# Performance work log

Measured on AMD Instinct MI355X. Metric: run time of the kernel, lower is better.

Reference implementation:

```python
import jax, jax.numpy as jnp
import numpy as np

B, T, C = 4, 1024, 1024
H, G = 16, 1            # n_head, n_query_groups
D = C // H              # head_dim = 64
E, K = 4, 1             # moe_num_experts, moe_k
FF = 4 * C              # ffn/expert hidden = 4096
EPS = 1e-5


def setup_inputs() -> dict:
    key = jax.random.key(0)
    ks = jax.random.split(key, 24)
    w = lambda k, shape: (jax.random.normal(k, shape, jnp.float32) * 0.02)
    return {
        "x": jax.random.normal(ks[0], (B, T, C), jnp.float32),
        # attention (torch Linear weights stored as [in, out])
        "wq": w(ks[1], (C, C)), "wk": w(ks[2], (C, C)), "wv": w(ks[3], (C, C)),
        "wo": w(ks[4], (C, C)), "bo": jnp.zeros((C,), jnp.float32),
        # feedforward
        "ff_w1": w(ks[5], (C, FF)), "ff_b1": jnp.zeros((FF,), jnp.float32),
        "ff_w2": w(ks[6], (FF, C)), "ff_b2": jnp.zeros((C,), jnp.float32),
        # MoE experts (stacked) + gate
        "exp_w1": w(ks[7], (E, C, FF)), "exp_b1": jnp.zeros((E, FF), jnp.float32),
        "exp_w2": w(ks[8], (E, FF, C)), "exp_b2": jnp.zeros((E, C), jnp.float32),
        "gate_w": w(ks[9], (C, E)), "gate_b": jnp.zeros((E,), jnp.float32),
        # layernorms
        "ln1_g": jnp.ones((C,), jnp.float32), "ln1_b": jnp.zeros((C,), jnp.float32),
        "ln2_g": jnp.ones((C,), jnp.float32), "ln2_b": jnp.zeros((C,), jnp.float32),
        "ln3_g": jnp.ones((C,), jnp.float32), "ln3_b": jnp.zeros((C,), jnp.float32),
    }


def _ln(x, g, b):
    m = x.mean(-1, keepdims=True)
    v = x.var(-1, keepdims=True)
    return (x - m) / jnp.sqrt(v + EPS) * g + b


def reference(x, wq, wk, wv, wo, bo, ff_w1, ff_b1, ff_w2, ff_b2,
              exp_w1, exp_b1, exp_w2, exp_b2, gate_w, gate_b,
              ln1_g, ln1_b, ln2_g, ln2_b, ln3_g, ln3_b):
    Hg = H // G
    # ---- grouped-query causal self-attention ----
    h = _ln(x, ln1_g, ln1_b)
    # [B,T,C] -> [B,G,Hg,T,D]
    q = (h @ wq).reshape(B, T, G, Hg, D).transpose(0, 2, 3, 1, 4)
    k = (h @ wk).reshape(B, T, G, Hg, D).transpose(0, 2, 3, 1, 4)
    v = (h @ wv).reshape(B, T, G, Hg, D).transpose(0, 2, 3, 1, 4)
    scores = jnp.einsum('bghtd,bghsd->bghts', q, k) / np.float32(np.sqrt(D))
    causal = jnp.tril(jnp.ones((T, T), bool))
    scores = jnp.where(causal, scores, -jnp.inf)
    probs = jax.nn.softmax(scores, axis=-1)
    o = jnp.einsum('bghts,bghsd->bghtd', probs, v)          # [B,G,Hg,T,D]
    o = o.reshape(B, H, T, D).transpose(0, 2, 1, 3).reshape(B, T, C)
    x = x + o @ wo + bo
    # ---- dense feedforward ----
    h = _ln(x, ln2_g, ln2_b)
    x = x + jax.nn.relu(h @ ff_w1 + ff_b1) @ ff_w2 + ff_b2
    # ---- MoE: compute ALL experts densely, gather top-k (faithful to source) ----
    h = _ln(x, ln3_g, ln3_b)
    gate = h @ gate_w + gate_b                               # [B,T,E]
    topk_s, topk_i = jax.lax.top_k(gate, K)                  # [B,T,K]
    topk_w = jax.nn.softmax(topk_s, axis=-1)
    hidden = jax.nn.relu(jnp.einsum('btc,ech->bteh', h, exp_w1) + exp_b1)
    expert_out = jnp.einsum('bteh,ehc->btec', hidden, exp_w2) + exp_b2  # [B,T,E,C]
    sel = jnp.take_along_axis(expert_out, topk_i[..., None], axis=2)    # [B,T,K,C]
    moe = (sel * topk_w[..., None]).sum(axis=2)
    return x + moe
```

## Files before the change

### kernel.cpp

```cpp
#include <hip/hip_runtime.h>


using f16   = _Float16;
using f16x4 = __attribute__((ext_vector_type(4))) _Float16;
using f16x8 = __attribute__((ext_vector_type(8))) _Float16;
using f32x4 = __attribute__((ext_vector_type(4))) float;

__device__ __forceinline__ void async16(void* l, const void* g) {
  __builtin_amdgcn_global_load_lds(
      (const __attribute__((address_space(1))) unsigned*)g,
      (__attribute__((address_space(3))) unsigned*)l, 16, 0, 0);
}

template <bool SPLITW>
__global__ __launch_bounds__(256) void transpose_k(
    const float* __restrict__ in, f16* __restrict__ oh, f16* __restrict__ ol,
    int R, int Cc) {
  const size_t bofs = (size_t)blockIdx.y * R * Cc;
  in += bofs; oh += bofs;
  if constexpr (SPLITW) ol += bofs;
  __shared__ float tile[32][33];
  const int nbx = Cc >> 5;
  const int bx = blockIdx.x % nbx, by = blockIdx.x / nbx;
  const int tx = threadIdx.x & 31, ty = threadIdx.x >> 5;
#pragma unroll
  for (int i = 0; i < 4; ++i) {
    int r = ty + i * 8;
    tile[r][tx] = in[(size_t)(by * 32 + r) * Cc + bx * 32 + tx];
  }
  __syncthreads();
#pragma unroll
  for (int i = 0; i < 4; ++i) {
    int oc = ty + i * 8;
    float v = tile[tx][oc];
    size_t o = (size_t)(bx * 32 + oc) * R + by * 32 + tx;
    f16 hi = (f16)v;
    oh[o] = hi;
    if constexpr (SPLITW) ol[o] = (f16)(v - (float)hi);
  }
}

__global__ __launch_bounds__(256) void ln_k(
    const float* __restrict__ x, const float* __restrict__ g,
    const float* __restrict__ b, f16* __restrict__ outh, f16* __restrict__ outl) {
  const int row = blockIdx.x;
  const float4 vv = ((const float4*)(x + (size_t)row * 1024))[threadIdx.x];
  float s = vv.x + vv.y + vv.z + vv.w;
  float sq = vv.x * vv.x + vv.y * vv.y + vv.z * vv.z + vv.w * vv.w;
#pragma unroll
  for (int mm = 32; mm; mm >>= 1) { s += __shfl_xor(s, mm); sq += __shfl_xor(sq, mm); }
  __shared__ float red[8];
  const int wv = threadIdx.x >> 6;
  if ((threadIdx.x & 63) == 0) { red[wv] = s; red[4 + wv] = sq; }
  __syncthreads();
  s = red[0] + red[1] + red[2] + red[3];
  sq = red[4] + red[5] + red[6] + red[7];
  const float mean = s * 0.0009765625f;
  const float rstd = rsqrtf(sq * 0.0009765625f - mean * mean + 1e-5f);
  const int c = threadIdx.x * 4;
  const float xs[4] = {vv.x, vv.y, vv.z, vv.w};
  f16x4 ovh, ovl;
#pragma unroll
  for (int i = 0; i < 4; ++i) {
    float val = (xs[i] - mean) * rstd * g[c + i] + b[c + i];
    f16 hi = (f16)val;
    ovh[i] = hi;
    ovl[i] = (f16)(val - (float)hi);
  }
  *(f16x4*)(outh + (size_t)row * 1024 + c) = ovh;
  *(f16x4*)(outl + (size_t)row * 1024 + c) = ovl;
}

__global__ __launch_bounds__(256) void gate_k(
    const float* __restrict__ x, const float* __restrict__ g, const float* __restrict__ b,
    const float* __restrict__ gw, const float* __restrict__ gb,
    int* __restrict__ cnt, int* __restrict__ idxAll, int* __restrict__ eid) {
  const int t = blockIdx.x;
  const float4 vv = ((const float4*)(x + (size_t)t * 1024))[threadIdx.x];
  float s = vv.x + vv.y + vv.z + vv.w;
  float sq = vv.x * vv.x + vv.y * vv.y + vv.z * vv.z + vv.w * vv.w;
#pragma unroll
  for (int mm = 32; mm; mm >>= 1) { s += __shfl_xor(s, mm); sq += __shfl_xor(sq, mm); }
  __shared__ float red[8];
  __shared__ float redv[4][4];
  const int wv = threadIdx.x >> 6;
  if ((threadIdx.x & 63) == 0) { red[wv] = s; red[4 + wv] = sq; }
  __syncthreads();
  s = red[0] + red[1] + red[2] + red[3];
  sq = red[4] + red[5] + red[6] + red[7];
  const float mean = s * 0.0009765625f;
  const float rstd = rsqrtf(sq * 0.0009765625f - mean * mean + 1e-5f);
  const int c = threadIdx.x * 4;
  const float xs[4] = {vv.x, vv.y, vv.z, vv.w};
  float a0 = 0.f, a1 = 0.f, a2 = 0.f, a3 = 0.f;
#pragma unroll
  for (int i = 0; i < 4; ++i) {
    float ln = (xs[i] - mean) * rstd * g[c + i] + b[c + i];
    const float4 w4 = ((const float4*)gw)[c + i];
    a0 += ln * w4.x; a1 += ln * w4.y; a2 += ln * w4.z; a3 += ln * w4.w;
  }
#pragma unroll
  for (int mm = 32; mm; mm >>= 1) {
    a0 += __shfl_xor(a0, mm); a1 += __shfl_xor(a1, mm);
    a2 += __shfl_xor(a2, mm); a3 += __shfl_xor(a3, mm);
  }
  if ((threadIdx.x & 63) == 0) {
    redv[wv][0] = a0; redv[wv][1] = a1; redv[wv][2] = a2; redv[wv][3] = a3;
  }
  __syncthreads();
  if (threadIdx.x == 0) {
    float ge[4];
#pragma unroll
    for (int e = 0; e < 4; ++e)
      ge[e] = redv[0][e] + redv[1][e] + redv[2][e] + redv[3][e] + gb[e];
    int be = 0; float bvv = ge[0];
#pragma unroll
    for (int e = 1; e < 4; ++e) if (ge[e] > bvv) { bvv = ge[e]; be = e; }
    int pos = atomicAdd(&cnt[be], 1);
    idxAll[(be << 12) + pos] = t;
    eid[t] = be;
  }
}

__global__ void init_moe(int* cnt) { if (threadIdx.x < 4) cnt[threadIdx.x] = 0; }

#define MAXMT 36
__global__ void plan_k(const int* __restrict__ cnt, int* __restrict__ desc) {
  if (threadIdx.x == 0) {
    int t = 0;
    for (int e = 0; e < 4; ++e) {
      const int c = cnt[e];
      for (int m = 0; m < c; m += 128) desc[t++] = (e << 16) | (m >> 7);
    }
    for (; t < MAXMT; ++t) desc[t] = -1;
  }
}

template <bool MOE>
__global__ __launch_bounds__(256) void reduce_k(
    const float* __restrict__ p0, const float* __restrict__ p1,
    const float* __restrict__ res, const float* __restrict__ bias,
    const int* __restrict__ eid, float* __restrict__ o) {
  const int row = blockIdx.x, t = threadIdx.x;
  const float* bp = MOE ? bias + (size_t)eid[row] * 1024 : bias;
  const float4 a = ((const float4*)(p0 + (size_t)row * 1024))[t];
  const float4 b = ((const float4*)(p1 + (size_t)row * 1024))[t];
  const float4 r = ((const float4*)(res + (size_t)row * 1024))[t];
  const float4 bb = ((const float4*)bp)[t];
  float4 o4;
  o4.x = r.x + a.x + b.x + bb.x;
  o4.y = r.y + a.y + b.y + bb.y;
  o4.z = r.z + a.z + b.z + bb.z;
  o4.w = r.w + a.w + b.w + bb.w;
  ((float4*)(o + (size_t)row * 1024))[t] = o4;
}

template <bool SPLIT, bool RELU, bool BIAS, bool RES, bool GATHER, int OUT,
          bool QKV3, bool KSPLIT>
__global__ __launch_bounds__(256, 2) void gemm_k(
    const f16* __restrict__ Ah, const f16* __restrict__ Al,
    const f16* __restrict__ Bh, const f16* __restrict__ Bl,
    float* __restrict__ outf, float* __restrict__ outf2,
    f16* __restrict__ outh, f16* __restrict__ outl,
    const float* __restrict__ bias, const float* __restrict__ res,
    const int* __restrict__ idxAll, const int* __restrict__ cntAll,
    const int* __restrict__ desc,
    int M, int N, int K) {
  const int NB = N >> 7;
  int m0, n0, ks = 0;
  int cnt = M;
  const int* idx = nullptr;
  if constexpr (GATHER) {
    int rem = blockIdx.x;
    if constexpr (KSPLIT) {
      const int half = (int)gridDim.x >> 1;
      ks = rem >= half; rem -= ks * half;
    }
    const int mt = rem / NB, nt = rem - mt * NB;
    const int d = desc[mt];
    if (d < 0) return;
    const int e = d >> 16;
    m0 = (d & 0xffff) << 7;
    n0 = nt << 7;
    cnt = cntAll[e];
    idx = idxAll + (e << 12);
    Bh += (size_t)e * N * K;
    if (BIAS) bias += (size_t)e * N;
  } else {
    int rem = blockIdx.x;
    const int ntile = (int)gridDim.x >> (KSPLIT ? 1 : 0);
    if constexpr (KSPLIT) { ks = rem >= ntile; rem -= ks * ntile; }
    const int q2 = ntile >> 3;
    const int bid = (rem & 7) * q2 + (rem >> 3);
    m0 = (bid / NB) << 7; n0 = (bid % NB) << 7;
  }

  __shared__ __align__(16) char lds[65536];

  const int tid = threadIdx.x;
  const int wave = tid >> 6, lane = tid & 63;
  const int wr = (wave >> 1) << 6, wc = (wave & 1) << 6;
  const int srow = lane >> 3;
  const int lc = (lane & 7) ^ srow;
  const int kofs = (SPLIT ? (lc >> 1) : lc) << 4;

  const int kshift = (KSPLIT && ks) ? (K >> 1) : 0;

  const char* srcA[4];
  const char* srcB[4];
#pragma unroll
  for (int s = 0; s < 4; ++s) {
    const int tr = (wave * 4 + s) * 8 + srow;
    int gm = m0 + tr;
    if constexpr (GATHER) gm = idx[gm < cnt ? gm : cnt - 1];
    const f16* baseA = (SPLIT && (lc & 1)) ? Al : Ah;
    srcA[s] = (const char*)baseA + ((size_t)gm * K + kshift) * 2 + kofs;
    const f16* baseB = (SPLIT && (lc & 1)) ? Bl : Bh;
    srcB[s] = (const char*)baseB + ((size_t)(n0 + tr) * K + kshift) * 2 + kofs;
  }
  char* const ldsw = lds + wave * 4096;

  const int s4 = lane >> 4, l7 = lane & 7, fr = lane & 15;
  int offAh[4], offAl[4], offBh[4], offBl[4];
#pragma unroll
  for (int i = 0; i < 4; ++i) {
    const int row = wr + i * 16 + fr;
    const int col = wc + i * 16 + fr;
    if constexpr (SPLIT) {
      offAh[i] = row * 128 + (((2 * s4) ^ l7) << 4);
      offAl[i] = row * 128 + (((2 * s4 + 1) ^ l7) << 4);
      offBh[i] = 16384 + col * 128 + (((2 * s4) ^ l7) << 4);
      offBl[i] = 16384 + col * 128 + (((2 * s4 + 1) ^ l7) << 4);
    } else {
      offAh[i] = row * 128 + ((s4 ^ l7) << 4);
      offAl[i] = row * 128 + (((4 + s4) ^ l7) << 4);
      offBh[i] = 16384 + col * 128 + ((s4 ^ l7) << 4);
      offBl[i] = 16384 + col * 128 + (((4 + s4) ^ l7) << 4);
    }
  }

  f32x4 acc[4][4] = {};

  constexpr int KSTEP = SPLIT ? 32 : 64;
  const int nt_ = (KSPLIT ? (K >> 1) : K) / KSTEP;

#pragma unroll
  for (int s = 0; s < 4; ++s) {
    async16(ldsw + s * 1024, srcA[s]);
    async16(ldsw + 16384 + s * 1024, srcB[s]);
  }

  for (int t = 0; t < nt_; ++t) {
    const int cur = t & 1;
    if (t + 1 < nt_) {
      const size_t kb = (size_t)(t + 1) * (KSTEP * 2);
      char* dst = ldsw + (cur ^ 1) * 32768;
#pragma unroll
      for (int s = 0; s < 4; ++s) {
        async16(dst + s * 1024, srcA[s] + kb);
        async16(dst + 16384 + s * 1024, srcB[s] + kb);
      }
      asm volatile("s_waitcnt vmcnt(8)" ::: "memory");
    } else {
      asm volatile("s_waitcnt vmcnt(0)" ::: "memory");
    }
    __builtin_amdgcn_s_barrier();
    __builtin_amdgcn_sched_barrier(0);

    const char* cab = lds + cur * 32768;
    f16x8 va[4], vb[4], va2[4], vb2[4];
#pragma unroll
    for (int i = 0; i < 4; ++i) {
      va[i]  = *(const f16x8*)(cab + offAh[i]);
      va2[i] = *(const f16x8*)(cab + offAl[i]);
      vb[i]  = *(const f16x8*)(cab + offBh[i]);
      vb2[i] = *(const f16x8*)(cab + offBl[i]);
    }
    __builtin_amdgcn_s_setprio(1);
#pragma unroll
    for (int i = 0; i < 4; ++i)
#pragma unroll
      for (int j = 0; j < 4; ++j) {
        if constexpr (SPLIT) {
          acc[i][j] = __builtin_amdgcn_mfma_f32_16x16x32_f16(va[i],  vb[j],  acc[i][j], 0, 0, 0);
          acc[i][j] = __builtin_amdgcn_mfma_f32_16x16x32_f16(va2[i], vb[j],  acc[i][j], 0, 0, 0);
          acc[i][j] = __builtin_amdgcn_mfma_f32_16x16x32_f16(va[i],  vb2[j], acc[i][j], 0, 0, 0);
        } else {
          acc[i][j] = __builtin_amdgcn_mfma_f32_16x16x32_f16(va[i],  vb[j],  acc[i][j], 0, 0, 0);
          acc[i][j] = __builtin_amdgcn_mfma_f32_16x16x32_f16(va2[i], vb2[j], acc[i][j], 0, 0, 0);
        }
      }
    __builtin_amdgcn_s_setprio(0);
    __builtin_amdgcn_sched_barrier(0);
    __builtin_amdgcn_s_barrier();
  }

  const int cl = lane & 15, rg = lane >> 4;
  float* const po = (OUT == 3) ? (ks ? outf2 : outf) : outf;
#pragma unroll
  for (int i = 0; i < 4; ++i) {
#pragma unroll
    for (int r = 0; r < 4; ++r) {
      const int mloc = m0 + wr + i * 16 + rg * 4 + r;
      if (GATHER && mloc >= cnt) continue;
      const int orow = GATHER ? idx[mloc] : mloc;
#pragma unroll
      for (int j = 0; j < 4; ++j) {
        const int col = n0 + wc + j * 16 + cl;
        float v2 = acc[i][j][r];
        if (BIAS) v2 += bias[col];
        if (RELU) v2 = v2 > 0.f ? v2 : 0.f;
        if (RES) v2 += res[(size_t)orow * N + col];
        size_t oidx;
        if constexpr (QKV3) {
          if (col < 2048) {
            oidx = ((size_t)(col >> 10) * M + orow) * 1024 + (col & 1023);
          } else {
            const int c = col - 2048;
            oidx = (size_t)2 * M * 1024 +
                   (((size_t)(orow >> 10) * 16 + (c >> 6)) * 64 + (c & 63)) * 1024 +
                   (orow & 1023);
          }
        } else {
          oidx = (size_t)orow * N + col;
        }
        if constexpr (OUT == 0 || OUT == 3) {
          po[oidx] = v2;
        } else if constexpr (OUT == 1) {
          f16 hi = (f16)v2;
          outh[oidx] = hi;
          outl[oidx] = (f16)(v2 - (float)hi);
        } else {
          outh[oidx] = (f16)v2;
        }
      }
    }
  }
}

__global__ __launch_bounds__(256, 3) void attn_k(
    const f16* __restrict__ qh, const f16* __restrict__ ql,
    const f16* __restrict__ kh, const f16* __restrict__ kl,
    const f16* __restrict__ vth, const f16* __restrict__ vtl,
    f16* __restrict__ oh, f16* __restrict__ ol) {
  const int qt = 15 - (blockIdx.x & 15), hd = (blockIdx.x >> 4) & 15, bb = blockIdx.x >> 8;
  const int tid = threadIdx.x, wave = tid >> 6, lane = tid & 63;
  __shared__ __align__(16) char QPs[16384], Ks[16384], Vs[16384];
  const int swz = (((lane & 7) ^ ((lane >> 3) & 7)) << 4);
  const size_t tok0 = (size_t)bb * 1024;
  const int hoff = hd * 64;
  const size_t vbase = ((size_t)(bb * 16 + hd) * 64) * 1024;
  const float L2E = 1.44269504089f;

#pragma unroll
  for (int r = 0; r < 2; ++r) {
    const int chunk = wave * 2 + r;
    const int row = chunk * 8 + (lane >> 3);
    const size_t byte = (((tok0 + qt * 64 + row) * 1024 + hoff) << 1) + swz;
    async16(QPs + chunk * 1024, (const char*)qh + byte);
    async16(QPs + 8192 + chunk * 1024, (const char*)ql + byte);
  }
  __syncthreads();
  f16x8 qr_h[2], qr_l[2];
#pragma unroll
  for (int ks = 0; ks < 2; ++ks) {
    const int qrow = wave * 16 + (lane & 15);
    const int qoff = qrow * 128 + ((((ks << 2) + (lane >> 4)) ^ (qrow & 7)) << 4);
    qr_h[ks] = *(const f16x8*)(QPs + qoff);
    qr_l[ks] = *(const f16x8*)(QPs + 8192 + qoff);
  }

  f32x4 oacc[4] = {};
  float mrun[4] = {-1e30f, -1e30f, -1e30f, -1e30f};
  float lrun[4] = {};

  for (int kt = 0; kt <= qt; ++kt) {
    __syncthreads();
#pragma unroll
    for (int r = 0; r < 2; ++r) {
      const int chunk = wave * 2 + r;
      const int row = chunk * 8 + (lane >> 3);
      const size_t kbyte = (((tok0 + kt * 64 + row) * 1024 + hoff) << 1) + swz;
      async16(Ks + chunk * 1024, (const char*)kh + kbyte);
      async16(Ks + 8192 + chunk * 1024, (const char*)kl + kbyte);
      const size_t vbyte = (((vbase + (size_t)row * 1024) + kt * 64) << 1) + swz;
      async16(Vs + chunk * 1024, (const char*)vth + vbyte);
      async16(Vs + 8192 + chunk * 1024, (const char*)vtl + vbyte);
    }
    __syncthreads();

    f32x4 s[4] = {};
#pragma unroll
    for (int ks = 0; ks < 2; ++ks) {
#pragma unroll
      for (int j = 0; j < 4; ++j) {
        const int col = j * 16 + (lane & 15);
        const int koff = col * 128 + ((((ks << 2) + (lane >> 4)) ^ (col & 7)) << 4);
        f16x8 b_h = *(const f16x8*)(Ks + koff);
        f16x8 b_l = *(const f16x8*)(Ks + 8192 + koff);
        s[j] = __builtin_amdgcn_mfma_f32_16x16x32_f16(qr_h[ks], b_h, s[j], 0, 0, 0);
        s[j] = __builtin_amdgcn_mfma_f32_16x16x32_f16(qr_l[ks], b_h, s[j], 0, 0, 0);
        s[j] = __builtin_amdgcn_mfma_f32_16x16x32_f16(qr_h[ks], b_l, s[j], 0, 0, 0);
      }
    }

    const bool diag = (kt == qt);
    float pmax[4] = {-1e30f, -1e30f, -1e30f, -1e30f};
#pragma unroll
    for (int j = 0; j < 4; ++j)
#pragma unroll
      for (int r = 0; r < 4; ++r) {
        float sv = s[j][r] * 0.125f;
        if (diag) {
          const int qloc = wave * 16 + (lane >> 4) * 4 + r;
          const int kvl = j * 16 + (lane & 15);
          if (kvl > qloc) sv = -1e30f;
        }
        s[j][r] = sv;
        pmax[r] = fmaxf(pmax[r], sv);
      }
    char* pbh = QPs + wave * 2048;
    char* pbl = QPs + 8192 + wave * 2048;
#pragma unroll
    for (int r = 0; r < 4; ++r) {
#pragma unroll
      for (int mm = 1; mm < 16; mm <<= 1)
        pmax[r] = fmaxf(pmax[r], __shfl_xor(pmax[r], mm, 16));
      const float mnew = fmaxf(mrun[r], pmax[r]);
      const float al = exp2f((mrun[r] - mnew) * L2E);
      mrun[r] = mnew;
      lrun[r] *= al;
      oacc[0][r] *= al; oacc[1][r] *= al; oacc[2][r] *= al; oacc[3][r] *= al;
    }

    float psum[4] = {};
#pragma unroll
    for (int j = 0; j < 4; ++j)
#pragma unroll
      for (int r = 0; r < 4; ++r) {
        const float p = exp2f((s[j][r] - mrun[r]) * L2E);
        psum[r] += p;
        const int lr = (lane >> 4) * 4 + r;
        const int kvl = j * 16 + (lane & 15);
        const int poff = lr * 128 + ((kvl * 2) ^ ((lr & 7) << 4));
        f16 ph = (f16)p;
        *(f16*)(pbh + poff) = ph;
        *(f16*)(pbl + poff) = (f16)(p - (float)ph);
      }
#pragma unroll
    for (int r = 0; r < 4; ++r) {
#pragma unroll
      for (int mm = 1; mm < 16; mm <<= 1)
        psum[r] += __shfl_xor(psum[r], mm, 16);
      lrun[r] += psum[r];
    }

#pragma unroll
    for (int ks = 0; ks < 2; ++ks) {
      const int prow = lane & 15;
      const int poff = prow * 128 + ((((ks << 2) + (lane >> 4)) ^ (prow & 7)) << 4);
      f16x8 a_h = *(const f16x8*)(pbh + poff);
      f16x8 a_l = *(const f16x8*)(pbl + poff);
#pragma unroll
      for (int jd = 0; jd < 4; ++jd) {
        const int col = jd * 16 + (lane & 15);
        const int voff = col * 128 + ((((ks << 2) + (lane >> 4)) ^ (col & 7)) << 4);
        f16x8 b_h = *(const f16x8*)(Vs + voff);
        f16x8 b_l = *(const f16x8*)(Vs + 8192 + voff);
        oacc[jd] = __builtin_amdgcn_mfma_f32_16x16x32_f16(a_h, b_h, oacc[jd], 0, 0, 0);
        oacc[jd] = __builtin_amdgcn_mfma_f32_16x16x32_f16(a_l, b_h, oacc[jd], 0, 0, 0);
        oacc[jd] = __builtin_amdgcn_mfma_f32_16x16x32_f16(a_h, b_l, oacc[jd], 0, 0, 0);
      }
    }
  }

#pragma unroll
  for (int r = 0; r < 4; ++r) {
    const float inv = 1.0f / lrun[r];
    const size_t trow = tok0 + qt * 64 + wave * 16 + (lane >> 4) * 4 + r;
#pragma unroll
    for (int jd = 0; jd < 4; ++jd) {
      const int col = hoff + jd * 16 + (lane & 15);
      const float val = oacc[jd][r] * inv;
      const f16 hi = (f16)val;
      oh[trow * 1024 + col] = hi;
      ol[trow * 1024 + col] = (f16)(val - (float)hi);
    }
  }
}

extern "C" void kernel_launch(void* const* d_in, const int* in_sizes, int n_in,
                              void* d_out, int out_size, void* d_ws, size_t ws_size,
                              hipStream_t stream) {
  const float* x0   = (const float*)d_in[0];
  const float* wq   = (const float*)d_in[1];
  const float* wk   = (const float*)d_in[2];
  const float* wv   = (const float*)d_in[3];
  const float* wo   = (const float*)d_in[4];
  const float* bo   = (const float*)d_in[5];
  const float* ffw1 = (const float*)d_in[6];
  const float* ffb1 = (const float*)d_in[7];
  const float* ffw2 = (const float*)d_in[8];
  const float* ffb2 = (const float*)d_in[9];
  const float* ew1  = (const float*)d_in[10];
  const float* eb1  = (const float*)d_in[11];
  const float* ew2  = (const float*)d_in[12];
  const float* eb2  = (const float*)d_in[13];
  const float* gw   = (const float*)d_in[14];
  const float* gb   = (const float*)d_in[15];
  const float* l1g  = (const float*)d_in[16];
  const float* l1b  = (const float*)d_in[17];
  const float* l2g  = (const float*)d_in[18];
  const float* l2b  = (const float*)d_in[19];
  const float* l3g  = (const float*)d_in[20];
  const float* l3b  = (const float*)d_in[21];
  float* out = (float*)d_out;

  char* w = (char*)d_ws;
  const size_t M1 = (size_t)1024 * 1024;
  const size_t A1 = (size_t)4096 * 1024 * 2;
  const size_t W4 = (size_t)1024 * 4096 * 2;
  f16* wqkvh = (f16*)w; w += 3 * M1 * 2;
  f16* wqkvl = (f16*)w; w += 3 * M1 * 2;
  f16* woh = (f16*)w; w += M1 * 2;
  f16* wol = (f16*)w; w += M1 * 2;
  f16* f1h = (f16*)w; w += W4;  f16* f1l = (f16*)w; w += W4;
  f16* f2h = (f16*)w; w += W4;  f16* f2l = (f16*)w; w += W4;
  f16* e1t = (f16*)w; w += 4 * W4;
  f16* e2t = (f16*)w; w += 4 * W4;
  f16* hh  = (f16*)w; w += A1;  f16* hl  = (f16*)w; w += A1;
  f16* qkv_h = (f16*)w; w += 3 * A1;
  f16* qkv_l = (f16*)w; w += 3 * A1;
  f16* o_h = (f16*)w; w += A1;  f16* o_l = (f16*)w; w += A1;
  float* x1 = (float*)w; w += (size_t)4096 * 1024 * 4;
  int* cnt = (int*)w; w += 256;
  int* idx = (int*)w; w += (size_t)4 * 4096 * 4;
  int* eid = (int*)w; w += (size_t)4096 * 4;
  int* desc = (int*)w; w += 256;
  f16* hid_h = qkv_h;
  f16* hid_l = (f16*)((char*)qkv_h + (((size_t)32) << 20));
  f16* ffh   = qkv_h;
  float* pW0 = (float*)hh;
  float* pW1 = (float*)qkv_h;
  float* pF0 = (float*)wqkvh;
  float* pF1 = (float*)hh;
  float* pM0 = (float*)((char*)qkv_l + (((size_t)8) << 20));
  float* pM1 = (float*)o_h;

  transpose_k<true><<<1024, 256, 0, stream>>>(wq, wqkvh, wqkvl, 1024, 1024);
  transpose_k<true><<<1024, 256, 0, stream>>>(wk, wqkvh + M1, wqkvl + M1, 1024, 1024);
  transpose_k<true><<<1024, 256, 0, stream>>>(wv, wqkvh + 2 * M1, wqkvl + 2 * M1, 1024, 1024);
  transpose_k<true><<<1024, 256, 0, stream>>>(wo, woh, wol, 1024, 1024);
  transpose_k<true><<<4096, 256, 0, stream>>>(ffw1, f1h, f1l, 1024, 4096);
  transpose_k<true><<<4096, 256, 0, stream>>>(ffw2, f2h, f2l, 4096, 1024);
  transpose_k<false><<<dim3(4096, 4), 256, 0, stream>>>(ew1, e1t, nullptr, 1024, 4096);
  transpose_k<false><<<dim3(4096, 4), 256, 0, stream>>>(ew2, e2t, nullptr, 4096, 1024);

  const size_t TOK = (size_t)4096 * 1024;
  ln_k<<<4096, 256, 0, stream>>>(x0, l1g, l1b, hh, hl);
  gemm_k<true, false, false, false, false, 1, true, false><<<768, 256, 0, stream>>>(
      hh, hl, wqkvh, wqkvl, nullptr, nullptr, qkv_h, qkv_l,
      nullptr, nullptr, nullptr, nullptr, nullptr, 4096, 3072, 1024);
  attn_k<<<1024, 256, 0, stream>>>(qkv_h, qkv_l, qkv_h + TOK, qkv_l + TOK,
                                   qkv_h + 2 * TOK, qkv_l + 2 * TOK, o_h, o_l);
  gemm_k<true, false, false, false, false, 3, false, true><<<512, 256, 0, stream>>>(
      o_h, o_l, woh, wol, pW0, pW1, nullptr, nullptr,
      nullptr, nullptr, nullptr, nullptr, nullptr, 4096, 1024, 1024);
  reduce_k<false><<<4096, 256, 0, stream>>>(pW0, pW1, x0, bo, nullptr, x1);

  ln_k<<<4096, 256, 0, stream>>>(x1, l2g, l2b, hh, hl);
  gemm_k<true, true, true, false, false, 1, false, false><<<1024, 256, 0, stream>>>(
      hh, hl, f1h, f1l, nullptr, nullptr, hid_h, hid_l,
      ffb1, nullptr, nullptr, nullptr, nullptr, 4096, 4096, 1024);
  gemm_k<true, false, false, false, false, 3, false, true><<<512, 256, 0, stream>>>(
      hid_h, hid_l, f2h, f2l, pF0, pF1, nullptr, nullptr,
      nullptr, nullptr, nullptr, nullptr, nullptr, 4096, 1024, 4096);
  reduce_k<false><<<4096, 256, 0, stream>>>(pF0, pF1, x1, ffb2, nullptr, out);

  ln_k<<<4096, 256, 0, stream>>>(out, l3g, l3b, hh, hl);
  init_moe<<<1, 64, 0, stream>>>(cnt);
  gate_k<<<4096, 256, 0, stream>>>(out, l3g, l3b, gw, gb, cnt, idx, eid);
  plan_k<<<1, 64, 0, stream>>>(cnt, desc);
  gemm_k<false, true, true, false, true, 2, false, false><<<MAXMT * 32, 256, 0, stream>>>(
      hh, nullptr, e1t, nullptr, nullptr, nullptr, ffh, nullptr,
      eb1, nullptr, idx, cnt, desc, 4096, 4096, 1024);
  gemm_k<false, false, false, false, true, 3, false, true><<<2 * MAXMT * 8, 256, 0, stream>>>(
      ffh, nullptr, e2t, nullptr, pM0, pM1, nullptr, nullptr,
      nullptr, nullptr, idx, cnt, desc, 4096, 1024, 4096);
  reduce_k<true><<<4096, 256, 0, stream>>>(pM0, pM1, out, eb2, eid, out);
}
```

Baseline: 793.1 us.

## Drop GEMM LDS double buffering to single buffer for higher occupancy

Removes the double-buffered async prefetch in the GEMM main loop and uses one 32 KB LDS buffer, loading each K-step and syncing before compute. Launch bounds rise to 4 blocks per CU so more waves can hide memory latency instead of software pipelining. The trade-off is losing overlap of global loads with MFMA within a block. It also relies on __syncthreads waiting for the global_load_lds transfers, which the removed explicit vmcnt waits used to guarantee, and 4 blocks of 256 threads may not fit under the register budget.

```diff
diff --git a/kernel.cpp b/kernel.cpp
--- a/kernel.cpp
+++ b/kernel.cpp
@@ -157,7 +157,7 @@
 
 template <bool SPLIT, bool RELU, bool BIAS, bool RES, bool GATHER, int OUT,
           bool QKV3, bool KSPLIT>
-__global__ __launch_bounds__(256, 2) void gemm_k(
+__global__ __launch_bounds__(256, 4) void gemm_k(
     const f16* __restrict__ Ah, const f16* __restrict__ Al,
     const f16* __restrict__ Bh, const f16* __restrict__ Bl,
     float* __restrict__ outf, float* __restrict__ outf2,
@@ -195,7 +195,7 @@
     m0 = (bid / NB) << 7; n0 = (bid % NB) << 7;
   }
 
-  __shared__ __align__(16) char lds[65536];
+  __shared__ __align__(16) char lds[32768];
 
   const int tid = threadIdx.x;
   const int wave = tid >> 6, lane = tid & 63;
@@ -244,37 +244,22 @@
   constexpr int KSTEP = SPLIT ? 32 : 64;
   const int nt_ = (KSPLIT ? (K >> 1) : K) / KSTEP;
 
-#pragma unroll
-  for (int s = 0; s < 4; ++s) {
-    async16(ldsw + s * 1024, srcA[s]);
-    async16(ldsw + 16384 + s * 1024, srcB[s]);
-  }
-
   for (int t = 0; t < nt_; ++t) {
-    const int cur = t & 1;
-    if (t + 1 < nt_) {
-      const size_t kb = (size_t)(t + 1) * (KSTEP * 2);
-      char* dst = ldsw + (cur ^ 1) * 32768;
-#pragma unroll
-      for (int s = 0; s < 4; ++s) {
-        async16(dst + s * 1024, srcA[s] + kb);
-        async16(dst + 16384 + s * 1024, srcB[s] + kb);
-      }
-      asm volatile("s_waitcnt vmcnt(8)" ::: "memory");
-    } else {
-      asm volatile("s_waitcnt vmcnt(0)" ::: "memory");
-    }
-    __builtin_amdgcn_s_barrier();
-    __builtin_amdgcn_sched_barrier(0);
-
-    const char* cab = lds + cur * 32768;
+    const size_t kb = (size_t)t * (KSTEP * 2);
+#pragma unroll
+    for (int s = 0; s < 4; ++s) {
+      async16(ldsw + s * 1024, srcA[s] + kb);
+      async16(ldsw + 16384 + s * 1024, srcB[s] + kb);
+    }
+    __syncthreads();
+
     f16x8 va[4], vb[4], va2[4], vb2[4];
 #pragma unroll
     for (int i = 0; i < 4; ++i) {
-      va[i]  = *(const f16x8*)(cab + offAh[i]);
-      va2[i] = *(const f16x8*)(cab + offAl[i]);
-      vb[i]  = *(const f16x8*)(cab + offBh[i]);
-      vb2[i] = *(const f16x8*)(cab + offBl[i]);
+      va[i]  = *(const f16x8*)(lds + offAh[i]);
+      va2[i] = *(const f16x8*)(lds + offAl[i]);
+      vb[i]  = *(const f16x8*)(lds + offBh[i]);
+      vb2[i] = *(const f16x8*)(lds + offBl[i]);
     }
     __builtin_amdgcn_s_setprio(1);
 #pragma unroll
@@ -291,8 +276,7 @@
         }
       }
     __builtin_amdgcn_s_setprio(0);
-    __builtin_amdgcn_sched_barrier(0);
-    __builtin_amdgcn_s_barrier();
+    __syncthreads();
   }
 
   const int cl = lane & 15, rg = lane >> 4;
```

Result: slower. 1.655 ms (+108.7%).
